# Kernel tuning notes

Measured on AMD Instinct MI355X. Metric: run time of the kernel, lower is better.

## Reference

```python
import jax, jax.numpy as jnp
import numpy as np

W_DIM = 512   # latent dim
CH = 512      # number of Fourier channels / output channels
SIZE = 64     # spatial size (square: size[0]=size[1])
SR = 64.0     # sampling_rate
BW = 2.0      # bandwidth
BATCH = 32


def setup_inputs() -> dict:
    key = jax.random.key(0)
    k1, k2, k3, k4, k5 = jax.random.split(key, 5)
    w = jax.random.normal(k1, (BATCH, W_DIM), jnp.float32)
    # affine FC params (weight_init=0 in original; use small random so t varies)
    affine_w = jax.random.normal(k2, (4, W_DIM), jnp.float32) * 0.1
    affine_b = jnp.array([1.0, 0.0, 0.0, 0.0], jnp.float32)
    # channel-mixing weight
    weight = jax.random.normal(k3, (CH, CH), jnp.float32)
    # freqs buffer init: randn, normalized by r*exp(r^2/4), scaled by bandwidth
    f = jax.random.normal(k4, (CH, 2), jnp.float32)
    radii = jnp.sqrt(jnp.sum(f * f, axis=1, keepdims=True))
    f = f / (radii * jnp.exp(radii * radii / 4.0)) * BW
    phases = jax.random.uniform(k5, (CH,), jnp.float32) - 0.5
    return {"w": w, "affine_w": affine_w, "affine_b": affine_b,
            "weight": weight, "freqs": f, "phases": phases}


def reference(w, affine_w, affine_b, weight, freqs, phases):
    # affine FC: FullyConnectedLayer with lr_multiplier=1 -> weight_gain = 1/sqrt(in)
    gain = np.float32(1.0 / np.sqrt(W_DIM))
    t = w @ (affine_w.T * gain) + affine_b                      # [N, 4]
    t = t / jnp.linalg.norm(t[:, :2], axis=1, keepdims=True)
    c, s, tx, ty = t[:, 0], t[:, 1], t[:, 2], t[:, 3]
    # combined transform = m_r @ m_t @ I; top-left 2x2 rotation block:
    R = jnp.stack([jnp.stack([c, -s], -1),
                   jnp.stack([s, c], -1)], axis=1)              # [N, 2, 2]
    # translation column of combined transform (m_r @ m_t)[:, :2, 2]
    trans = jnp.stack([-c * tx + s * ty, -s * tx - c * ty], -1) # [N, 2]
    ph = phases[None, :] + jnp.einsum('cd,nd->nc', freqs, trans)  # [N, C]
    fr = jnp.einsum('cd,nde->nce', freqs, R)                      # [N, C, 2]
    amp = jnp.clip(1.0 - (jnp.linalg.norm(fr, axis=2) - BW) / (SR / 2.0 - BW), 0.0, 1.0)  # [N, C]
    # affine_grid(theta, [1,1,H,W], align_corners=False): base coords (2i+1)/D - 1
    scale = np.float32(0.5 * SIZE / SR)
    xs = ((2.0 * jnp.arange(SIZE, dtype=jnp.float32) + 1.0) / SIZE - 1.0) * scale
    ys = ((2.0 * jnp.arange(SIZE, dtype=jnp.float32) + 1.0) / SIZE - 1.0) * scale
    grid = jnp.stack([jnp.broadcast_to(xs[None, :], (SIZE, SIZE)),
                      jnp.broadcast_to(ys[:, None], (SIZE, SIZE))], axis=-1)  # [H, W, 2]
    # per-pixel Fourier phase: [N, H, W, C]
    x = jnp.einsum('hwd,ncd->nhwc', grid, fr) + ph[:, None, None, :]
    x = jnp.sin(x * np.float32(2.0 * np.pi)) * amp[:, None, None, :]
    # channel projection, then to NCHW
    x = jnp.einsum('nhwc,kc->nkhw', x, weight * np.float32(1.0 / np.sqrt(CH)))
    return x  # [N, CH, H, W]
```

## Files before the change

### kernel.cpp

```cpp
#include <hip/hip_runtime.h>
#include <hip/hip_bf16.h>

#define WDIM 512
#define CHN  512
#define NB   32
#define SZ   64
#define MTOT 4096

typedef __attribute__((ext_vector_type(4))) float f32x4;
typedef __attribute__((ext_vector_type(8))) short short8;
typedef __attribute__((ext_vector_type(4))) int   int4v;
typedef __attribute__((ext_vector_type(4))) unsigned int uint4v;

__device__ __forceinline__ unsigned pack_bf(float a, float b) {
    union { __hip_bfloat16 h; unsigned short u; } x, y;
    x.h = __float2bfloat16(a); y.h = __float2bfloat16(b);
    return (unsigned)x.u | ((unsigned)y.u << 16);
}
__device__ __forceinline__ float lo16f(unsigned u) {
    union { unsigned x; float f; } t; t.x = u << 16; return t.f;
}
__device__ __forceinline__ float hi16f(unsigned u) {
    union { unsigned x; float f; } t; t.x = u & 0xffff0000u; return t.f;
}

__global__ __launch_bounds__(512) void prep_kernel(
    const float* __restrict__ win,
    const float* __restrict__ affine_w,
    const float* __restrict__ affine_b,
    const float* __restrict__ freqs,
    const float* __restrict__ phases,
    const float* __restrict__ wsrc,
    unsigned* __restrict__ SCA, unsigned* __restrict__ SCB,
    __hip_bfloat16* __restrict__ wbf)
{
    const int b = blockIdx.x;
    const int tid = threadIdx.x;
    if (b < NB * 64) {
        const int n = b >> 6;
        const int w = b & 63;
        __shared__ float red[8][4];
        __shared__ float par[4];

        float wv = win[n * WDIM + tid];
        float p0 = wv * affine_w[0 * WDIM + tid];
        float p1 = wv * affine_w[1 * WDIM + tid];
        float p2 = wv * affine_w[2 * WDIM + tid];
        float p3 = wv * affine_w[3 * WDIM + tid];
        #pragma unroll
        for (int off = 32; off >= 1; off >>= 1) {
            p0 += __shfl_down(p0, off);
            p1 += __shfl_down(p1, off);
            p2 += __shfl_down(p2, off);
            p3 += __shfl_down(p3, off);
        }
        const int wave = tid >> 6;
        if ((tid & 63) == 0) {
            red[wave][0] = p0; red[wave][1] = p1;
            red[wave][2] = p2; red[wave][3] = p3;
        }
        __syncthreads();
        if (tid == 0) {
            const float gain = 0.04419417382415922f;
            float t[4];
            #pragma unroll
            for (int j = 0; j < 4; ++j) {
                float s = 0.0f;
                #pragma unroll
                for (int v = 0; v < 8; ++v) s += red[v][j];
                t[j] = s * gain + affine_b[j];
            }
            float inv = 1.0f / sqrtf(t[0] * t[0] + t[1] * t[1]);
            float c = t[0] * inv, s = t[1] * inv, tx = t[2] * inv, ty = t[3] * inv;
            par[0] = c;
            par[1] = s;
            par[2] = -c * tx + s * ty;
            par[3] = -s * tx - c * ty;
        }
        __syncthreads();
        const float c_ = par[0], s_ = par[1], tr0 = par[2], tr1 = par[3];
        const int c = tid;
        float fx = freqs[c * 2 + 0], fy = freqs[c * 2 + 1];
        float frx = fx * c_ + fy * s_;
        float fry = -fx * s_ + fy * c_;
        float ph = phases[c] + fx * tr0 + fy * tr1;
        float r = sqrtf(frx * frx + fry * fry);
        float amp = 1.0f - (r - 2.0f) * (1.0f / 30.0f);
        amp = fminf(fmaxf(amp, 0.0f), 1.0f);
        float xs = (float)(2 * w + 1) * (1.0f / 128.0f) - 0.5f;
        size_t idx = ((size_t)(n * 64 + w)) * CHN + c;
        float sA = amp * __builtin_amdgcn_sinf(xs * frx);
        float cA = amp * __builtin_amdgcn_cosf(xs * frx);
        float bb = xs * fry + ph;
        SCA[idx] = pack_bf(sA, cA);
        SCB[idx] = pack_bf(__builtin_amdgcn_sinf(bb), __builtin_amdgcn_cosf(bb));
    } else {
        int i = (b - NB * 64) * 512 + tid;
        wbf[i] = __float2bfloat16(wsrc[i] * 0.04419417382415922f);
    }
}

__global__ __launch_bounds__(256, 2) void fused_kernel(
    const unsigned* __restrict__ SCA, const unsigned* __restrict__ SCB,
    const __hip_bfloat16* __restrict__ wbf,
    float* __restrict__ out)
{
    __shared__ __align__(16) __hip_bfloat16 As[128 * 64];
    __shared__ __align__(16) __hip_bfloat16 Bs[256 * 64];

    const int bid  = blockIdx.x;
    const int orig = (bid & 7) * 256 + (bid >> 3);
    const int n  = orig >> 6;
    const int kb = ((orig >> 5) & 1) * 256;
    const int mb = (orig & 31) * 128;
    const int h0 = mb >> 6;

    const int tid = threadIdx.x;
    const int lane = tid & 63;
    const int wid  = tid >> 6;
    const int ln15 = lane & 15;
    const int hi4  = lane >> 4;
    const int wk   = wid * 64;

    const int cc0 = (tid & 7) * 8;
    const int rb  = tid >> 3;

    const unsigned* pA0 = SCA + ((size_t)(n * 64 + rb)) * CHN + cc0;
    const unsigned* pA1 = pA0 + 32 * CHN;
    const unsigned* pB0 = SCB + ((size_t)(n * 64 + h0)) * CHN + cc0;
    const unsigned* pB1 = pB0 + CHN;

    uint4v A00, A01, A10, A11, B00, B01, B10, B11;
    auto loadT = [&](int c0) {
        A00 = *(const uint4v*)(pA0 + c0); A01 = *(const uint4v*)(pA0 + c0 + 4);
        A10 = *(const uint4v*)(pA1 + c0); A11 = *(const uint4v*)(pA1 + c0 + 4);
        B00 = *(const uint4v*)(pB0 + c0); B01 = *(const uint4v*)(pB0 + c0 + 4);
        B10 = *(const uint4v*)(pB1 + c0); B11 = *(const uint4v*)(pB1 + c0 + 4);
    };

    f32x4 acc[4][8];
    #pragma unroll
    for (int a = 0; a < 4; ++a)
        #pragma unroll
        for (int b = 0; b < 8; ++b)
            acc[a][b] = (f32x4)0.0f;

    loadT(0);

    #pragma unroll 1
    for (int kc = 0; kc < 8; ++kc) {
        const int c0 = kc * 64;
        __syncthreads();

        #pragma unroll
        for (int u = 0; u < 8; ++u) {
            int unit = u * 256 + tid;
            int row = unit >> 3;
            int cbyte = ((unit & 7) << 4) ^ ((row & 7) << 4);
            const __hip_bfloat16* src = wbf + (size_t)(kb + row) * CHN + c0 + (cbyte >> 1);
            char* ldsbase = (char*)Bs + (u * 256 + (wid << 6)) * 16;
            __builtin_amdgcn_global_load_lds(
                (const __attribute__((address_space(1))) unsigned int*)src,
                (__attribute__((address_space(3))) unsigned int*)ldsbase, 16, 0, 0);
        }

        #pragma unroll
        for (int i = 0; i < 4; ++i) {
            int m = rb + i * 32;
            uint4v Aa = (i & 1) ? A10 : A00, Ab = (i & 1) ? A11 : A01;
            uint4v Ba = (i >> 1) ? B10 : B00, Bb = (i >> 1) ? B11 : B01;
            union { __hip_bfloat16 h[8]; int4v v; } t;
            #pragma unroll
            for (int j = 0; j < 4; ++j)
                t.h[j] = __float2bfloat16(
                    lo16f(Aa[j]) * hi16f(Ba[j]) + hi16f(Aa[j]) * lo16f(Ba[j]));
            #pragma unroll
            for (int j = 0; j < 4; ++j)
                t.h[4 + j] = __float2bfloat16(
                    lo16f(Ab[j]) * hi16f(Bb[j]) + hi16f(Ab[j]) * lo16f(Bb[j]));
            *(int4v*)((char*)As + m * 128 + ((cc0 * 2) ^ ((m & 7) << 4))) = t.v;
        }
        __syncthreads();

        #pragma unroll
        for (int kk = 0; kk < 2; ++kk) {
            short8 wf[4], ff[8];
            #pragma unroll
            for (int ki = 0; ki < 4; ++ki) {
                int row = wk + ki * 16 + ln15;
                wf[ki] = *(const short8*)((char*)Bs + row * 128 +
                          (((kk * 32 + hi4 * 8) * 2) ^ ((row & 7) << 4)));
            }
            #pragma unroll
            for (int mj = 0; mj < 8; ++mj) {
                int m = mj * 16 + ln15;
                ff[mj] = *(const short8*)((char*)As + m * 128 +
                          (((kk * 32 + hi4 * 8) * 2) ^ ((m & 7) << 4)));
            }
            if (kk == 0 && kc < 7)
                loadT(c0 + 64);
            __builtin_amdgcn_s_setprio(1);
            #pragma unroll
            for (int ki = 0; ki < 4; ++ki)
                #pragma unroll
                for (int mj = 0; mj < 8; ++mj)
                    acc[ki][mj] = __builtin_amdgcn_mfma_f32_16x16x32_bf16(
                        wf[ki], ff[mj], acc[ki][mj], 0, 0, 0);
            __builtin_amdgcn_s_setprio(0);
        }
    }

    #pragma unroll
    for (int ki = 0; ki < 4; ++ki) {
        #pragma unroll
        for (int mj = 0; mj < 8; ++mj) {
            int kg = kb + wk + ki * 16 + hi4 * 4;
            int mg = mb + mj * 16 + ln15;
            float* op = out + ((size_t)n * CHN + kg) * MTOT + mg;
            #pragma unroll
            for (int r = 0; r < 4; ++r)
                op[(size_t)r * MTOT] = acc[ki][mj][r];
        }
    }
}

extern "C" void kernel_launch(void* const* d_in, const int* in_sizes, int n_in,
                              void* d_out, int out_size, void* d_ws, size_t ws_size,
                              hipStream_t stream) {
    const float* w        = (const float*)d_in[0];
    const float* affine_w = (const float*)d_in[1];
    const float* affine_b = (const float*)d_in[2];
    const float* weight   = (const float*)d_in[3];
    const float* freqs    = (const float*)d_in[4];
    const float* phases   = (const float*)d_in[5];
    float* out = (float*)d_out;

    char* ws = (char*)d_ws;
    __hip_bfloat16* wbf = (__hip_bfloat16*)(ws);
    unsigned* SCA = (unsigned*)(ws + (1u << 20));
    unsigned* SCB = (unsigned*)(ws + (1u << 20) + (4u << 20));

    prep_kernel<<<NB * 64 + (CHN * CHN) / 512, 512, 0, stream>>>(
        w, affine_w, affine_b, freqs, phases, weight, SCA, SCB, wbf);

    fused_kernel<<<2048, 256, 0, stream>>>(SCA, SCB, wbf, out);
}
```

Before: 105.3 us.

## Double-buffer weight tiles in LDS and prefetch two stages ahead

Splits the weight LDS tile into two buffers. The async global-to-LDS copy for stage k+2 is issued while stage k+1 features are being built, so the weight load overlaps MFMA work instead of sitting between barriers. The prologue stages the first two tiles, and each iteration uses explicit sched barriers with an lgkmcnt wait. This raises LDS use per block to about 80KB, which may limit two blocks per CU. Correctness relies on in-order vmcnt completion, which the wait on the register loads implies, rather than on an explicit vmcnt wait inside the loop.

```diff
diff --git a/kernel.cpp b/kernel.cpp
--- a/kernel.cpp
+++ b/kernel.cpp
@@ -22,6 +22,13 @@
 }
 __device__ __forceinline__ float hi16f(unsigned u) {
     union { unsigned x; float f; } t; t.x = u & 0xffff0000u; return t.f;
+}
+
+__device__ __forceinline__ void bar_lgkm() {
+    __builtin_amdgcn_sched_barrier(0);
+    asm volatile("s_waitcnt lgkmcnt(0)" ::: "memory");
+    __builtin_amdgcn_s_barrier();
+    __builtin_amdgcn_sched_barrier(0);
 }
 
 __global__ __launch_bounds__(512) void prep_kernel(
@@ -106,7 +113,7 @@
     float* __restrict__ out)
 {
     __shared__ __align__(16) __hip_bfloat16 As[128 * 64];
-    __shared__ __align__(16) __hip_bfloat16 Bs[256 * 64];
+    __shared__ __align__(16) __hip_bfloat16 Bs[2][256 * 64];
 
     const int bid  = blockIdx.x;
     const int orig = (bid & 7) * 256 + (bid >> 3);
@@ -129,6 +136,22 @@
     const unsigned* pA1 = pA0 + 32 * CHN;
     const unsigned* pB0 = SCB + ((size_t)(n * 64 + h0)) * CHN + cc0;
     const unsigned* pB1 = pB0 + CHN;
+
+    auto stageB = [&](int t) {
+        const int c0 = t * 64;
+        char* base = (char*)Bs[t & 1];
+        #pragma unroll
+        for (int u = 0; u < 8; ++u) {
+            int unit = u * 256 + tid;
+            int row = unit >> 3;
+            int cbyte = ((unit & 7) << 4) ^ ((row & 7) << 4);
+            const __hip_bfloat16* src = wbf + (size_t)(kb + row) * CHN + c0 + (cbyte >> 1);
+            char* ldsbase = base + (u * 256 + (wid << 6)) * 16;
+            __builtin_amdgcn_global_load_lds(
+                (const __attribute__((address_space(1))) unsigned int*)src,
+                (__attribute__((address_space(3))) unsigned int*)ldsbase, 16, 0, 0);
+        }
+    };
 
     uint4v A00, A01, A10, A11, B00, B01, B10, B11;
     auto loadT = [&](int c0) {
@@ -138,32 +161,7 @@
         B10 = *(const uint4v*)(pB1 + c0); B11 = *(const uint4v*)(pB1 + c0 + 4);
     };
 
-    f32x4 acc[4][8];
-    #pragma unroll
-    for (int a = 0; a < 4; ++a)
-        #pragma unroll
-        for (int b = 0; b < 8; ++b)
-            acc[a][b] = (f32x4)0.0f;
-
-    loadT(0);
-
-    #pragma unroll 1
-    for (int kc = 0; kc < 8; ++kc) {
-        const int c0 = kc * 64;
-        __syncthreads();
-
-        #pragma unroll
-        for (int u = 0; u < 8; ++u) {
-            int unit = u * 256 + tid;
-            int row = unit >> 3;
-            int cbyte = ((unit & 7) << 4) ^ ((row & 7) << 4);
-            const __hip_bfloat16* src = wbf + (size_t)(kb + row) * CHN + c0 + (cbyte >> 1);
-            char* ldsbase = (char*)Bs + (u * 256 + (wid << 6)) * 16;
-            __builtin_amdgcn_global_load_lds(
-                (const __attribute__((address_space(1))) unsigned int*)src,
-                (__attribute__((address_space(3))) unsigned int*)ldsbase, 16, 0, 0);
-        }
-
+    auto features = [&](int c0) {
         #pragma unroll
         for (int i = 0; i < 4; ++i) {
             int m = rb + i * 32;
@@ -180,15 +178,35 @@
                     lo16f(Ab[j]) * hi16f(Bb[j]) + hi16f(Ab[j]) * lo16f(Bb[j]));
             *(int4v*)((char*)As + m * 128 + ((cc0 * 2) ^ ((m & 7) << 4))) = t.v;
         }
-        __syncthreads();
-
+    };
+
+    f32x4 acc[4][8];
+    #pragma unroll
+    for (int a = 0; a < 4; ++a)
+        #pragma unroll
+        for (int b = 0; b < 8; ++b)
+            acc[a][b] = (f32x4)0.0f;
+
+    loadT(0);
+    stageB(0);
+    features(0);
+    stageB(1);
+    __builtin_amdgcn_sched_barrier(0);
+    asm volatile("s_waitcnt lgkmcnt(0)" ::: "memory");
+    asm volatile("s_waitcnt vmcnt(8)" ::: "memory");
+    __builtin_amdgcn_s_barrier();
+    __builtin_amdgcn_sched_barrier(0);
+
+    #pragma unroll 1
+    for (int kc = 0; kc < 8; ++kc) {
+        const char* bsbase = (const char*)Bs[kc & 1];
         #pragma unroll
         for (int kk = 0; kk < 2; ++kk) {
             short8 wf[4], ff[8];
             #pragma unroll
             for (int ki = 0; ki < 4; ++ki) {
                 int row = wk + ki * 16 + ln15;
-                wf[ki] = *(const short8*)((char*)Bs + row * 128 +
+                wf[ki] = *(const short8*)(bsbase + row * 128 +
                           (((kk * 32 + hi4 * 8) * 2) ^ ((row & 7) << 4)));
             }
             #pragma unroll
@@ -198,7 +216,7 @@
                           (((kk * 32 + hi4 * 8) * 2) ^ ((m & 7) << 4)));
             }
             if (kk == 0 && kc < 7)
-                loadT(c0 + 64);
+                loadT((kc + 1) * 64);
             __builtin_amdgcn_s_setprio(1);
             #pragma unroll
             for (int ki = 0; ki < 4; ++ki)
@@ -208,6 +226,11 @@
                         wf[ki], ff[mj], acc[ki][mj], 0, 0, 0);
             __builtin_amdgcn_s_setprio(0);
         }
+
+        bar_lgkm();
+        if (kc < 7) features((kc + 1) * 64);
+        if (kc < 6) stageB(kc + 2);
+        bar_lgkm();
     }
 
     #pragma unroll
```

After: 111.3 us. 5.7% more time.
